# Kernel tuning notes

Measured on AMD Instinct MI355X. Metric: run time of the kernel, lower is better.

## Reference

```python
import jax, jax.numpy as jnp
import numpy as np

D = 1024      # model_dim
H = 2048      # expert hidden_dim
E = 8         # num routed experts
TOP_K = 2
N_SHARED = 1
B, S = 2, 1024


def setup_inputs() -> dict:
    key = jax.random.key(0)
    ks = jax.random.split(key, 12)
    sc = 0.02
    return {
        "hidden": jax.random.normal(ks[0], (B, S, D), jnp.float32),
        # router Linear(D -> E); stored as [in, out]
        "router_w": jax.random.normal(ks[1], (D, E), jnp.float32) * sc,
        "router_b": jnp.zeros((E,), jnp.float32),
        # shared expert (1): Linear(D->H), Linear(H->D)
        "sw1": jax.random.normal(ks[2], (D, H), jnp.float32) * sc,
        "sb1": jnp.zeros((H,), jnp.float32),
        "sw2": jax.random.normal(ks[3], (H, D), jnp.float32) * sc,
        "sb2": jnp.zeros((D,), jnp.float32),
        # routed experts, stacked over E
        "rw1": jax.random.normal(ks[4], (E, D, H), jnp.float32) * sc,
        "rb1": jnp.zeros((E, H), jnp.float32),
        "rw2": jax.random.normal(ks[5], (E, H, D), jnp.float32) * sc,
        "rb2": jnp.zeros((E, D), jnp.float32),
    }


def reference(hidden, router_w, router_b, sw1, sb1, sw2, sb2, rw1, rb1, rw2, rb2):
    b, s, d = hidden.shape
    T = b * s
    flat = hidden.reshape(T, d)                              # [T, D]

    # --- router ---
    router_logits = flat @ router_w + router_b               # [T, E]
    router_probs = jax.nn.softmax(router_logits, axis=-1)
    topk_probs, topk_idx = jax.lax.top_k(router_probs, TOP_K)  # [T, K]

    # per-(token, expert) mixing weight: sum of top-k probs that hit expert e
    weights = jnp.zeros_like(router_probs).at[
        jnp.arange(T)[:, None], topk_idx
    ].add(topk_probs)                                        # [T, E]

    # --- shared expert(s) (1 expert -> mean == itself) ---
    sh = jax.nn.gelu(flat @ sw1 + sb1, approximate=False)    # [T, H]
    shared_out = (sh @ sw2 + sb2) / N_SHARED                 # [T, D]

    # --- routed experts: dense all-expert eval weighted by routing weights ---
    # (identical math to the gather/FFN/index_add loop: weight is 0 for
    #  tokens not routed to expert e)
    h1 = jax.nn.gelu(jnp.einsum('td,edh->teh', flat, rw1) + rb1[None],
                     approximate=False)                      # [T, E, H]
    expert_out = jnp.einsum('teh,ehd->ted', h1, rw2) + rb2[None]  # [T, E, D]
    mixed = jnp.einsum('ted,te->td', expert_out, weights)    # [T, D]

    return (shared_out + mixed).reshape(b, s, d)
```

## Files before the change

kernel.cpp:

```cpp
#include <hip/hip_runtime.h>
#include <hip/hip_bf16.h>

#define T_TOK 2048
#define DDIM  1024
#define HDIM  2048
#define NEXP  8
#define NSEG  9

typedef unsigned short u16;
typedef __attribute__((ext_vector_type(4))) float f32x4;
typedef __attribute__((ext_vector_type(8))) short bf16x8;
typedef __attribute__((ext_vector_type(4))) unsigned short u16x4;

__device__ __forceinline__ u16 f2bf(float x) {
  union { float f; unsigned int u; } v; v.f = x;
  unsigned int r = v.u + 0x7fffu + ((v.u >> 16) & 1u);
  return (u16)(r >> 16);
}
__device__ __forceinline__ float gelu_exact(float x) {
  return 0.5f * x * (1.0f + erff(x * 0.70710678118654752f));
}
__device__ __forceinline__ int swz4(int row) {
  return (row & 3) ^ ((row >> 2) & 3);
}

__device__ __forceinline__ void gload16(const void* g, void* l) {
  __builtin_amdgcn_global_load_lds(
      (const __attribute__((address_space(1))) unsigned int*)g,
      (__attribute__((address_space(3))) unsigned int*)l, 16, 0, 0);
}

__global__ __launch_bounds__(256) void router_kernel(
    const float* __restrict__ x, const float* __restrict__ rw,
    const float* __restrict__ rb, u16* __restrict__ xb,
    float* __restrict__ weights, int* __restrict__ counts,
    int* __restrict__ lists)
{
  int wv = threadIdx.x >> 6, lane = threadIdx.x & 63;
  int t = blockIdx.x * 4 + wv;
  const float* xrow = x + (size_t)t * DDIM;
  float acc[NEXP];
#pragma unroll
  for (int e = 0; e < NEXP; e++) acc[e] = 0.f;
#pragma unroll
  for (int i = 0; i < 4; i++) {
    int d0 = i * 256 + lane * 4;
    f32x4 xv = *(const f32x4*)(xrow + d0);
    u16x4 pk;
#pragma unroll
    for (int j = 0; j < 4; j++) {
      float xs = xv[j];
      pk[j] = f2bf(xs);
      const float* wr = rw + (size_t)(d0 + j) * NEXP;
#pragma unroll
      for (int e = 0; e < NEXP; e++) acc[e] = fmaf(xs, wr[e], acc[e]);
    }
    *(u16x4*)(xb + (size_t)t * DDIM + d0) = pk;
  }
#pragma unroll
  for (int off = 32; off >= 1; off >>= 1)
#pragma unroll
    for (int e = 0; e < NEXP; e++) acc[e] += __shfl_xor(acc[e], off);

  if (lane == 0) {
    float lg[NEXP], mx = -1e30f;
#pragma unroll
    for (int e = 0; e < NEXP; e++) { lg[e] = acc[e] + rb[e]; mx = fmaxf(mx, lg[e]); }
    float p[NEXP], s = 0.f;
#pragma unroll
    for (int e = 0; e < NEXP; e++) { p[e] = expf(lg[e] - mx); s += p[e]; }
    float inv = 1.0f / s;
#pragma unroll
    for (int e = 0; e < NEXP; e++) p[e] *= inv;
    int i1 = 0;
#pragma unroll
    for (int e = 1; e < NEXP; e++) if (p[e] > p[i1]) i1 = e;
    int i2 = (i1 == 0) ? 1 : 0;
#pragma unroll
    for (int e = 0; e < NEXP; e++) if (e != i1 && p[e] > p[i2]) i2 = e;
#pragma unroll
    for (int e = 0; e < NEXP; e++)
      weights[(size_t)t * NEXP + e] = (e == i1) ? p[i1] : (e == i2) ? p[i2] : 0.f;
    int p1 = atomicAdd(counts + i1, 1); lists[i1 * T_TOK + p1] = t;
    int p2 = atomicAdd(counts + i2, 1); lists[i2 * T_TOK + p2] = t;
    lists[NEXP * T_TOK + t] = t;
  }
}

__global__ void seg_kernel(int* counts, int* segoff, int* ytab, int* nyt) {
  counts[NEXP] = T_TOK;
  int off = 0, n = 0;
  for (int e = 0; e < NSEG; e++) {
    segoff[e] = off;
    int c = counts[e];
    for (int my = 0; my * 256 < c; my++) ytab[n++] = e * 256 + my;
    off += c;
  }
  *nyt = n;
}

__global__ __launch_bounds__(256) void transpose_bf16_kernel(
    const float* __restrict__ rin, const float* __restrict__ sin_,
    u16* __restrict__ rout, u16* __restrict__ sout, int R, int C)
{
  __shared__ float tile[32][33];
  int b = blockIdx.z;
  const float* inb = (b < NEXP) ? rin + (size_t)b * R * C : sin_;
  u16* outb = (b < NEXP) ? rout + (size_t)b * R * C : sout;
  int r0 = blockIdx.y * 32, c0 = blockIdx.x * 32;
  int tx = threadIdx.x & 31, ty = threadIdx.x >> 5;
#pragma unroll
  for (int j = 0; j < 4; j++) {
    int r = ty + j * 8;
    tile[r][tx] = inb[(size_t)(r0 + r) * C + c0 + tx];
  }
  __syncthreads();
#pragma unroll
  for (int j = 0; j < 4; j++) {
    int rr = ty + j * 8;
    outb[(size_t)(c0 + rr) * R + r0 + tx] = f2bf(tile[tx][rr]);
  }
}


__global__ __launch_bounds__(512) void gemm1_kernel(
    const u16* __restrict__ Xb, const u16* __restrict__ rw1t,
    const u16* __restrict__ sw1t, const float* __restrict__ rb1,
    const float* __restrict__ sb1, const int* __restrict__ counts,
    const int* __restrict__ segoff, const int* __restrict__ lists,
    const int* __restrict__ ytab, const int* __restrict__ nyt,
    u16* __restrict__ H1)
{
  __shared__ u16 Alds[2][256 * 32];
  __shared__ u16 Blds[2][256 * 32];

  int tid = threadIdx.x, lane = tid & 63;
  int wv = tid >> 6, wm = wv >> 2, wn = wv & 3;
  int kc = lane >> 4, lr = lane & 15;

  int srow[2], soff[2];
#pragma unroll
  for (int r = 0; r < 2; r++) {
    int i = r * 512 + tid;
    srow[r] = i >> 2;
    soff[r] = (((i & 3) ^ swz4(i >> 2)) * 8);
  }
  int aoff[8], boff[4];
#pragma unroll
  for (int f = 0; f < 8; f++) {
    int ra = wm * 128 + f * 16 + lr;
    aoff[f] = ra * 32 + ((kc ^ swz4(ra)) * 8);
  }
#pragma unroll
  for (int f = 0; f < 4; f++) {
    int rb_ = wn * 64 + f * 16 + lr;
    boff[f] = rb_ * 32 + ((kc ^ swz4(rb_)) * 8);
  }

  int ntile = nyt[0] * (HDIM / 256);
  for (int t = blockIdx.x; t < ntile; t += gridDim.x) {
    int yt = t >> 3, nx = t & 7;
    int em = ytab[yt];
    int e = em >> 8, m0 = (em & 255) * 256, n0 = nx * 256;
    int cnt = counts[e];
    const u16* Bt = (e < NEXP) ? (rw1t + (size_t)e * HDIM * DDIM) : sw1t;
    const float* bias = (e < NEXP) ? (rb1 + (size_t)e * HDIM) : sb1;
    const int* list = lists + e * T_TOK;
    int seg = segoff[e];

    size_t abase[2], bbase[2];
#pragma unroll
    for (int r = 0; r < 2; r++) {
      int tok = list[min(m0 + srow[r], cnt - 1)];
      abase[r] = (size_t)tok * DDIM + soff[r];
      bbase[r] = (size_t)(n0 + srow[r]) * DDIM + soff[r];
    }

    f32x4 acc[8][4];
#pragma unroll
    for (int i = 0; i < 8; i++)
#pragma unroll
      for (int j = 0; j < 4; j++) acc[i][j] = (f32x4){0.f, 0.f, 0.f, 0.f};

#pragma unroll
    for (int r = 0; r < 2; r++) {
      int i = r * 512 + tid;
      gload16(Xb + abase[r], &Alds[0][i * 8]);
      gload16(Bt + bbase[r], &Blds[0][i * 8]);
    }
    __syncthreads();

    const int NS = DDIM / 32;
    for (int s = 0; s < NS; s++) {
      int cur = s & 1;
      if (s + 1 < NS) {
        int kk = (s + 1) * 32;
#pragma unroll
        for (int r = 0; r < 2; r++) {
          int i = r * 512 + tid;
          gload16(Xb + abase[r] + kk, &Alds[cur ^ 1][i * 8]);
          gload16(Bt + bbase[r] + kk, &Blds[cur ^ 1][i * 8]);
        }
      }
      bf16x8 af[8], bfr[4];
#pragma unroll
      for (int f = 0; f < 8; f++) af[f] = *(const bf16x8*)(&Alds[cur][aoff[f]]);
#pragma unroll
      for (int f = 0; f < 4; f++) bfr[f] = *(const bf16x8*)(&Blds[cur][boff[f]]);
#pragma unroll
      for (int mf = 0; mf < 8; mf++)
#pragma unroll
        for (int nf = 0; nf < 4; nf++)
          acc[mf][nf] = __builtin_amdgcn_mfma_f32_16x16x32_bf16(af[mf], bfr[nf], acc[mf][nf], 0, 0, 0);
      __syncthreads();
    }

#pragma unroll
    for (int nf = 0; nf < 4; nf++) {
      int col = n0 + wn * 64 + nf * 16 + lr;
      float b = bias[col];
#pragma unroll
      for (int mf = 0; mf < 8; mf++) {
#pragma unroll
        for (int rg = 0; rg < 4; rg++) {
          int mt = wm * 128 + mf * 16 + (lane >> 4) * 4 + rg;
          if (m0 + mt < cnt) {
            float v = acc[mf][nf][rg] + b;
            H1[(size_t)(seg + m0 + mt) * HDIM + col] = f2bf(gelu_exact(v));
          }
        }
      }
    }
  }
}

__global__ __launch_bounds__(512) void gemm2_kernel(
    const u16* __restrict__ H1, const u16* __restrict__ rw2t,
    const u16* __restrict__ sw2t, const float* __restrict__ rb2,
    const float* __restrict__ sb2, const float* __restrict__ weights,
    const int* __restrict__ counts, const int* __restrict__ segoff,
    const int* __restrict__ lists, const int* __restrict__ ytab,
    const int* __restrict__ nyt, float* __restrict__ out)
{
  __shared__ u16 Alds[2][256 * 32];
  __shared__ u16 Blds[2][256 * 32];

  int tid = threadIdx.x, lane = tid & 63;
  int wv = tid >> 6, wm = wv >> 2, wn = wv & 3;
  int kc = lane >> 4, lr = lane & 15;

  int srow[2], soff[2];
#pragma unroll
  for (int r = 0; r < 2; r++) {
    int i = r * 512 + tid;
    srow[r] = i >> 2;
    soff[r] = (((i & 3) ^ swz4(i >> 2)) * 8);
  }
  int aoff[8], boff[4];
#pragma unroll
  for (int f = 0; f < 8; f++) {
    int ra = wm * 128 + f * 16 + lr;
    aoff[f] = ra * 32 + ((kc ^ swz4(ra)) * 8);
  }
#pragma unroll
  for (int f = 0; f < 4; f++) {
    int rb_ = wn * 64 + f * 16 + lr;
    boff[f] = rb_ * 32 + ((kc ^ swz4(rb_)) * 8);
  }

  int ntile = nyt[0] * (DDIM / 256) * 2;
  for (int t = blockIdx.x; t < ntile; t += gridDim.x) {
    int kh = t & 1, nx = (t >> 1) & 3, yt = t >> 3;
    int em = ytab[yt];
    int e = em >> 8, m0 = (em & 255) * 256, n0 = nx * 256;
    int cnt = counts[e];
    const u16* Bt = (e < NEXP) ? (rw2t + (size_t)e * DDIM * HDIM) : sw2t;
    const float* bias = (e < NEXP) ? (rb2 + (size_t)e * DDIM) : sb2;
    const int* list = lists + e * T_TOK;
    int seg = segoff[e];
    int k0 = kh * 1024;

    size_t abase[2], bbase[2];
#pragma unroll
    for (int r = 0; r < 2; r++) {
      abase[r] = (size_t)(seg + min(m0 + srow[r], cnt - 1)) * HDIM + k0 + soff[r];
      bbase[r] = (size_t)(n0 + srow[r]) * HDIM + k0 + soff[r];
    }

    f32x4 acc[8][4];
#pragma unroll
    for (int i = 0; i < 8; i++)
#pragma unroll
      for (int j = 0; j < 4; j++) acc[i][j] = (f32x4){0.f, 0.f, 0.f, 0.f};

#pragma unroll
    for (int r = 0; r < 2; r++) {
      int i = r * 512 + tid;
      gload16(H1 + abase[r], &Alds[0][i * 8]);
      gload16(Bt + bbase[r], &Blds[0][i * 8]);
    }
    __syncthreads();

    const int NS = 1024 / 32;
    for (int s = 0; s < NS; s++) {
      int cur = s & 1;
      if (s + 1 < NS) {
        int kk = (s + 1) * 32;
#pragma unroll
        for (int r = 0; r < 2; r++) {
          int i = r * 512 + tid;
          gload16(H1 + abase[r] + kk, &Alds[cur ^ 1][i * 8]);
          gload16(Bt + bbase[r] + kk, &Blds[cur ^ 1][i * 8]);
        }
      }
      bf16x8 af[8], bfr[4];
#pragma unroll
      for (int f = 0; f < 8; f++) af[f] = *(const bf16x8*)(&Alds[cur][aoff[f]]);
#pragma unroll
      for (int f = 0; f < 4; f++) bfr[f] = *(const bf16x8*)(&Blds[cur][boff[f]]);
#pragma unroll
      for (int mf = 0; mf < 8; mf++)
#pragma unroll
        for (int nf = 0; nf < 4; nf++)
          acc[mf][nf] = __builtin_amdgcn_mfma_f32_16x16x32_bf16(af[mf], bfr[nf], acc[mf][nf], 0, 0, 0);
      __syncthreads();
    }

    float biasv[4];
#pragma unroll
    for (int nf = 0; nf < 4; nf++)
      biasv[nf] = (kh == 0) ? bias[n0 + wn * 64 + nf * 16 + lr] : 0.f;

#pragma unroll
    for (int mf = 0; mf < 8; mf++) {
#pragma unroll
      for (int rg = 0; rg < 4; rg++) {
        int mt = wm * 128 + mf * 16 + (lane >> 4) * 4 + rg;
        int mrow = m0 + mt;
        if (mrow < cnt) {
          int tok = list[mrow];
          float w = (e < NEXP) ? weights[(size_t)tok * NEXP + e] : 1.0f;
          float* orow = out + (size_t)tok * DDIM + n0 + wn * 64 + lr;
#pragma unroll
          for (int nf = 0; nf < 4; nf++)
            atomicAdd(orow + nf * 16, w * (acc[mf][nf][rg] + biasv[nf]));
        }
      }
    }
  }
}

extern "C" void kernel_launch(void* const* d_in, const int* in_sizes, int n_in,
                              void* d_out, int out_size, void* d_ws, size_t ws_size,
                              hipStream_t stream) {
  (void)in_sizes; (void)n_in; (void)out_size; (void)ws_size;
  const float* hidden   = (const float*)d_in[0];
  const float* router_w = (const float*)d_in[1];
  const float* router_b = (const float*)d_in[2];
  const float* sw1 = (const float*)d_in[3];
  const float* sb1 = (const float*)d_in[4];
  const float* sw2 = (const float*)d_in[5];
  const float* sb2 = (const float*)d_in[6];
  const float* rw1 = (const float*)d_in[7];
  const float* rb1 = (const float*)d_in[8];
  const float* rw2 = (const float*)d_in[9];
  const float* rb2 = (const float*)d_in[10];
  float* out = (float*)d_out;

  char* ws = (char*)d_ws;
  u16* Xb      = (u16*)(ws + 0);
  u16* rw1t    = (u16*)(ws + 4194304);
  u16* rw2t    = (u16*)(ws + 37748736);
  u16* sw1t    = (u16*)(ws + 71303168);
  u16* sw2t    = (u16*)(ws + 75497472);
  u16* H1      = (u16*)(ws + 79691776);
  float* weights = (float*)(ws + 104857600);
  int* counts  = (int*)(ws + 104923136);
  int* segoff  = (int*)(ws + 104923200);
  int* lists   = (int*)(ws + 104923264);
  int* ytab    = (int*)(ws + 104996992);
  int* nyt     = (int*)(ws + 104997632);

  hipMemsetAsync(counts, 0, 64, stream);
  hipMemsetAsync(out, 0, (size_t)T_TOK * DDIM * sizeof(float), stream);

  router_kernel<<<T_TOK / 4, 256, 0, stream>>>(hidden, router_w, router_b, Xb,
                                               weights, counts, lists);
  seg_kernel<<<1, 1, 0, stream>>>(counts, segoff, ytab, nyt);

  transpose_bf16_kernel<<<dim3(HDIM / 32, DDIM / 32, NSEG), 256, 0, stream>>>(
      rw1, sw1, rw1t, sw1t, DDIM, HDIM);
  transpose_bf16_kernel<<<dim3(DDIM / 32, HDIM / 32, NSEG), 256, 0, stream>>>(
      rw2, sw2, rw2t, sw2t, HDIM, DDIM);

  gemm1_kernel<<<256, 512, 0, stream>>>(
      Xb, rw1t, sw1t, rb1, sb1, counts, segoff, lists, ytab, nyt, H1);
  gemm2_kernel<<<256, 512, 0, stream>>>(
      H1, rw2t, sw2t, rb2, sb2, weights, counts, segoff, lists, ytab, nyt, out);
}
```

Baseline: 264.9 us.

## Deepen GEMM LDS pipeline to four buffers with prefetch distance two

Both expert GEMM kernels move from a double-buffered LDS scheme with a full __syncthreads per K step to a four-buffer ring that prefetches two stages ahead. They wait on partial vmcnt counts and use a single s_barrier per step instead of draining all outstanding loads. MFMA sections are wrapped in s_setprio to favour the math waves. This doubles LDS use to 128 KB per block and relies on hand-tuned waitcnt values matching the number of direct-to-LDS loads, which is fragile if the load count changes.

```diff
diff --git a/kernel.cpp b/kernel.cpp
--- a/kernel.cpp
+++ b/kernel.cpp
@@ -131,8 +131,8 @@
     const int* __restrict__ ytab, const int* __restrict__ nyt,
     u16* __restrict__ H1)
 {
-  __shared__ u16 Alds[2][256 * 32];
-  __shared__ u16 Blds[2][256 * 32];
+  __shared__ u16 Alds[4][256 * 32];
+  __shared__ u16 Blds[4][256 * 32];
 
   int tid = threadIdx.x, lane = tid & 63;
   int wv = tid >> 6, wm = wv >> 2, wn = wv & 3;
@@ -140,10 +140,10 @@
 
   int srow[2], soff[2];
 #pragma unroll
-  for (int r = 0; r < 2; r++) {
-    int i = r * 512 + tid;
-    srow[r] = i >> 2;
-    soff[r] = (((i & 3) ^ swz4(i >> 2)) * 8);
+  for (int j = 0; j < 2; j++) {
+    int i = j * 512 + tid;
+    srow[j] = i >> 2;
+    soff[j] = (((i & 3) ^ swz4(i >> 2)) * 8);
   }
   int aoff[8], boff[4];
 #pragma unroll
@@ -170,10 +170,10 @@
 
     size_t abase[2], bbase[2];
 #pragma unroll
-    for (int r = 0; r < 2; r++) {
-      int tok = list[min(m0 + srow[r], cnt - 1)];
-      abase[r] = (size_t)tok * DDIM + soff[r];
-      bbase[r] = (size_t)(n0 + srow[r]) * DDIM + soff[r];
+    for (int j = 0; j < 2; j++) {
+      int tok = list[min(m0 + srow[j], cnt - 1)];
+      abase[j] = (size_t)tok * DDIM + soff[j];
+      bbase[j] = (size_t)(n0 + srow[j]) * DDIM + soff[j];
     }
 
     f32x4 acc[8][4];
@@ -182,37 +182,49 @@
 #pragma unroll
       for (int j = 0; j < 4; j++) acc[i][j] = (f32x4){0.f, 0.f, 0.f, 0.f};
 
-#pragma unroll
-    for (int r = 0; r < 2; r++) {
-      int i = r * 512 + tid;
-      gload16(Xb + abase[r], &Alds[0][i * 8]);
-      gload16(Bt + bbase[r], &Blds[0][i * 8]);
-    }
-    __syncthreads();
-
     const int NS = DDIM / 32;
+#pragma unroll
+    for (int s = 0; s < 2; s++)
+#pragma unroll
+      for (int j = 0; j < 2; j++) {
+        int i = j * 512 + tid;
+        gload16(Xb + abase[j] + s * 32, &Alds[s][i * 8]);
+        gload16(Bt + bbase[j] + s * 32, &Blds[s][i * 8]);
+      }
+
     for (int s = 0; s < NS; s++) {
-      int cur = s & 1;
-      if (s + 1 < NS) {
-        int kk = (s + 1) * 32;
-#pragma unroll
-        for (int r = 0; r < 2; r++) {
-          int i = r * 512 + tid;
-          gload16(Xb + abase[r] + kk, &Alds[cur ^ 1][i * 8]);
-          gload16(Bt + bbase[r] + kk, &Blds[cur ^ 1][i * 8]);
+      if (s + 2 < NS) {
+        int kk = (s + 2) * 32;
+        int nb = (s + 2) & 3;
+#pragma unroll
+        for (int j = 0; j < 2; j++) {
+          int i = j * 512 + tid;
+          gload16(Xb + abase[j] + kk, &Alds[nb][i * 8]);
+          gload16(Bt + bbase[j] + kk, &Blds[nb][i * 8]);
         }
-      }
+        asm volatile("s_waitcnt vmcnt(8)" ::: "memory");
+      } else if (s + 1 < NS) {
+        asm volatile("s_waitcnt vmcnt(4)" ::: "memory");
+      } else {
+        asm volatile("s_waitcnt vmcnt(0)" ::: "memory");
+      }
+      __builtin_amdgcn_s_barrier();
+      __builtin_amdgcn_sched_barrier(0);
+
+      const u16* Ac = &Alds[s & 3][0];
+      const u16* Bc = &Blds[s & 3][0];
       bf16x8 af[8], bfr[4];
 #pragma unroll
-      for (int f = 0; f < 8; f++) af[f] = *(const bf16x8*)(&Alds[cur][aoff[f]]);
-#pragma unroll
-      for (int f = 0; f < 4; f++) bfr[f] = *(const bf16x8*)(&Blds[cur][boff[f]]);
+      for (int f = 0; f < 8; f++) af[f] = *(const bf16x8*)(Ac + aoff[f]);
+#pragma unroll
+      for (int f = 0; f < 4; f++) bfr[f] = *(const bf16x8*)(Bc + boff[f]);
+      __builtin_amdgcn_s_setprio(1);
 #pragma unroll
       for (int mf = 0; mf < 8; mf++)
 #pragma unroll
         for (int nf = 0; nf < 4; nf++)
           acc[mf][nf] = __builtin_amdgcn_mfma_f32_16x16x32_bf16(af[mf], bfr[nf], acc[mf][nf], 0, 0, 0);
-      __syncthreads();
+      __builtin_amdgcn_s_setprio(0);
     }
 
 #pragma unroll
@@ -223,7 +235,7 @@
       for (int mf = 0; mf < 8; mf++) {
 #pragma unroll
         for (int rg = 0; rg < 4; rg++) {
-          int mt = wm * 128 + mf * 16 + (lane >> 4) * 4 + rg;
+          int mt = wm * 128 + mf * 16 + kc * 4 + rg;
           if (m0 + mt < cnt) {
             float v = acc[mf][nf][rg] + b;
             H1[(size_t)(seg + m0 + mt) * HDIM + col] = f2bf(gelu_exact(v));
@@ -231,6 +243,8 @@
         }
       }
     }
+    __builtin_amdgcn_s_barrier();
+    __builtin_amdgcn_sched_barrier(0);
   }
 }
 
@@ -242,8 +256,8 @@
     const int* __restrict__ lists, const int* __restrict__ ytab,
     const int* __restrict__ nyt, float* __restrict__ out)
 {
-  __shared__ u16 Alds[2][256 * 32];
-  __shared__ u16 Blds[2][256 * 32];
+  __shared__ u16 Alds[4][256 * 32];
+  __shared__ u16 Blds[4][256 * 32];
 
   int tid = threadIdx.x, lane = tid & 63;
   int wv = tid >> 6, wm = wv >> 2, wn = wv & 3;
@@ -251,10 +265,10 @@
 
   int srow[2], soff[2];
 #pragma unroll
-  for (int r = 0; r < 2; r++) {
-    int i = r * 512 + tid;
-    srow[r] = i >> 2;
-    soff[r] = (((i & 3) ^ swz4(i >> 2)) * 8);
+  for (int j = 0; j < 2; j++) {
+    int i = j * 512 + tid;
+    srow[j] = i >> 2;
+    soff[j] = (((i & 3) ^ swz4(i >> 2)) * 8);
   }
   int aoff[8], boff[4];
 #pragma unroll
@@ -282,9 +296,9 @@
 
     size_t abase[2], bbase[2];
 #pragma unroll
-    for (int r = 0; r < 2; r++) {
-      abase[r] = (size_t)(seg + min(m0 + srow[r], cnt - 1)) * HDIM + k0 + soff[r];
-      bbase[r] = (size_t)(n0 + srow[r]) * HDIM + k0 + soff[r];
+    for (int j = 0; j < 2; j++) {
+      abase[j] = (size_t)(seg + min(m0 + srow[j], cnt - 1)) * HDIM + k0 + soff[j];
+      bbase[j] = (size_t)(n0 + srow[j]) * HDIM + k0 + soff[j];
     }
 
     f32x4 acc[8][4];
@@ -293,37 +307,49 @@
 #pragma unroll
       for (int j = 0; j < 4; j++) acc[i][j] = (f32x4){0.f, 0.f, 0.f, 0.f};
 
-#pragma unroll
-    for (int r = 0; r < 2; r++) {
-      int i = r * 512 + tid;
-      gload16(H1 + abase[r], &Alds[0][i * 8]);
-      gload16(Bt + bbase[r], &Blds[0][i * 8]);
-    }
-    __syncthreads();
-
     const int NS = 1024 / 32;
+#pragma unroll
+    for (int s = 0; s < 2; s++)
+#pragma unroll
+      for (int j = 0; j < 2; j++) {
+        int i = j * 512 + tid;
+        gload16(H1 + abase[j] + s * 32, &Alds[s][i * 8]);
+        gload16(Bt + bbase[j] + s * 32, &Blds[s][i * 8]);
+      }
+
     for (int s = 0; s < NS; s++) {
-      int cur = s & 1;
-      if (s + 1 < NS) {
-        int kk = (s + 1) * 32;
-#pragma unroll
-        for (int r = 0; r < 2; r++) {
-          int i = r * 512 + tid;
-          gload16(H1 + abase[r] + kk, &Alds[cur ^ 1][i * 8]);
-          gload16(Bt + bbase[r] + kk, &Blds[cur ^ 1][i * 8]);
+      if (s + 2 < NS) {
+        int kk = (s + 2) * 32;
+        int nb = (s + 2) & 3;
+#pragma unroll
+        for (int j = 0; j < 2; j++) {
+          int i = j * 512 + tid;
+          gload16(H1 + abase[j] + kk, &Alds[nb][i * 8]);
+          gload16(Bt + bbase[j] + kk, &Blds[nb][i * 8]);
         }
-      }
+        asm volatile("s_waitcnt vmcnt(8)" ::: "memory");
+      } else if (s + 1 < NS) {
+        asm volatile("s_waitcnt vmcnt(4)" ::: "memory");
+      } else {
+        asm volatile("s_waitcnt vmcnt(0)" ::: "memory");
+      }
+      __builtin_amdgcn_s_barrier();
+      __builtin_amdgcn_sched_barrier(0);
+
+      const u16* Ac = &Alds[s & 3][0];
+      const u16* Bc = &Blds[s & 3][0];
       bf16x8 af[8], bfr[4];
 #pragma unroll
-      for (int f = 0; f < 8; f++) af[f] = *(const bf16x8*)(&Alds[cur][aoff[f]]);
-#pragma unroll
-      for (int f = 0; f < 4; f++) bfr[f] = *(const bf16x8*)(&Blds[cur][boff[f]]);
+      for (int f = 0; f < 8; f++) af[f] = *(const bf16x8*)(Ac + aoff[f]);
+#pragma unroll
+      for (int f = 0; f < 4; f++) bfr[f] = *(const bf16x8*)(Bc + boff[f]);
+      __builtin_amdgcn_s_setprio(1);
 #pragma unroll
       for (int mf = 0; mf < 8; mf++)
 #pragma unroll
         for (int nf = 0; nf < 4; nf++)
           acc[mf][nf] = __builtin_amdgcn_mfma_f32_16x16x32_bf16(af[mf], bfr[nf], acc[mf][nf], 0, 0, 0);
-      __syncthreads();
+      __builtin_amdgcn_s_setprio(0);
     }
 
     float biasv[4];
@@ -335,7 +361,7 @@
     for (int mf = 0; mf < 8; mf++) {
 #pragma unroll
       for (int rg = 0; rg < 4; rg++) {
-        int mt = wm * 128 + mf * 16 + (lane >> 4) * 4 + rg;
+        int mt = wm * 128 + mf * 16 + kc * 4 + rg;
         int mrow = m0 + mt;
         if (mrow < cnt) {
           int tok = list[mrow];
@@ -347,6 +373,8 @@
         }
       }
     }
+    __builtin_amdgcn_s_barrier();
+    __builtin_amdgcn_sched_barrier(0);
   }
 }
 
```

After: 248.9 us. -6.0%, faster.
